# Optimization experiments

Hardware: AMD Instinct MI355X
Metric: run time of the kernel (lower is better)

The kernel has to match this reference:

```python
import jax, jax.numpy as jnp
import numpy as np

NUM_JOINTS = 140
NUM_VERTICES = 13059
NUM_BONES = 28
BATCH = 512


def euler_zyx_to_rot(e):
    """e: [..., 3] Euler angles in (z, y, x) order -> [..., 3, 3] with R = Rz @ Ry @ Rx."""
    z, y, x = e[..., 0], e[..., 1], e[..., 2]
    cx, sx = jnp.cos(x), jnp.sin(x)
    cy, sy = jnp.cos(y), jnp.sin(y)
    cz, sz = jnp.cos(z), jnp.sin(z)
    r00 = cz * cy
    r01 = cz * sy * sx - sz * cx
    r02 = cz * sy * cx + sz * sx
    r10 = sz * cy
    r11 = sz * sy * sx + cz * cx
    r12 = sz * sy * cx - cz * sx
    r20 = -sy
    r21 = cy * sx
    r22 = cy * cx
    R = jnp.stack([r00, r01, r02, r10, r11, r12, r20, r21, r22], axis=-1)
    return R.reshape(e.shape[:-1] + (3, 3))


def _mouse_forward(pose, bone_lengths, center_bone_length, trans, scale,
                   v_template, t_pose_joints, weights, parent, bone_mapper):
    B = pose.shape[0]
    Jn = NUM_JOINTS
    dt = pose.dtype

    bl = jax.nn.sigmoid(bone_lengths / 5.0) * 2.0            # [B, 28]
    R = euler_zyx_to_rot(pose.reshape(B, Jn, 3))             # [B, J, 3, 3]
    Jt = t_pose_joints                                       # [J, 3]

    # bone offsets for joints 1..J-1, scaled per bone_length_mapper
    off = Jt[1:] - Jt[parent[1:]]                            # [J-1, 3]
    blid = bone_mapper[1:]                                   # [J-1]
    bl_g = jnp.where(blid[None, :] >= 0,
                     jnp.take(bl, jnp.maximum(blid, 0), axis=1),
                     jnp.ones((), dt))                       # [B, J-1]
    # joint index 1 (position 0 in the [J-1] arrays) uses center_bone_length
    scale_per = bl_g.at[:, 0].set(center_bone_length[:, 0])
    off_b = off[None] * scale_per[..., None]                 # [B, J-1, 3]

    bottom = jnp.broadcast_to(jnp.array([0., 0., 0., 1.], dt), (B, Jn - 1, 1, 4))
    top = jnp.concatenate([R[:, 1:], off_b[..., None]], axis=-1)   # [B, J-1, 3, 4]
    A = jnp.concatenate([top, bottom], axis=-2)              # [B, J-1, 4, 4] local transforms

    root_t = jnp.broadcast_to(Jt[0], (B, 3))[..., None]      # [B, 3, 1]
    root_top = jnp.concatenate([R[:, 0], root_t], axis=-1)   # [B, 3, 4]
    root_bot = jnp.broadcast_to(jnp.array([0., 0., 0., 1.], dt), (B, 1, 4))
    G0 = jnp.concatenate([root_top, root_bot], axis=-2)      # [B, 4, 4]

    G_init = jnp.zeros((B, Jn, 4, 4), dt).at[:, 0].set(G0)

    def step(G, xs):
        i, p, Ai = xs                                        # Ai: [B, 4, 4]
        Gp = jnp.take(G, p, axis=1)                          # [B, 4, 4]
        Gi = Gp @ Ai
        return G.at[:, i].set(Gi), None

    idx = jnp.arange(1, Jn)
    G, _ = jax.lax.scan(step, G_init, (idx, parent[1:], jnp.swapaxes(A, 0, 1)))

    J_final = G[:, :, :3, 3]                                 # [B, J, 3]

    # subtract rest-pose joint contribution (relative transforms for LBS)
    Jh = jnp.concatenate([jnp.broadcast_to(Jt, (B, Jn, 3)),
                          jnp.zeros((B, Jn, 1), dt)], axis=-1)      # [B, J, 4]
    d = jnp.einsum('bjmn,bjn->bjm', G, Jh)                   # [B, J, 4]
    G_rel = jnp.concatenate([G[..., :3], (G[..., 3] - d)[..., None]], axis=-1)

    # linear blend skinning
    T = jnp.einsum('vj,bjmn->bvmn', weights, G_rel)          # [B, V, 4, 4]
    vh = jnp.concatenate([v_template, jnp.ones((NUM_VERTICES, 1), dt)], axis=-1)
    V = jnp.einsum('bvmn,vn->bvm', T[:, :, :3, :], vh)       # [B, V, 3]

    s = scale[:, 0][:, None, None]
    V = V * s + trans[:, None, :]
    J_out = J_final * s + trans[:, None, :]
    return V, J_out


def setup_inputs() -> dict:
    key = jax.random.key(0)
    ks = jax.random.split(key, 8)
    rng = np.random.default_rng(0)
    parent = np.zeros(NUM_JOINTS, dtype=np.int32)
    for i in range(1, NUM_JOINTS):
        parent[i] = rng.integers(0, i)                       # valid kinematic tree
    bone_mapper = rng.integers(-1, NUM_BONES, size=NUM_JOINTS).astype(np.int32)
    W = jax.random.uniform(ks[6], (NUM_VERTICES, NUM_JOINTS), jnp.float32)
    W = W / jnp.sum(W, axis=1, keepdims=True)                # row-stochastic skinning weights
    return {
        'pose': jax.random.normal(ks[0], (BATCH, NUM_JOINTS * 3), jnp.float32) * 0.2,
        'bone_lengths': jax.random.normal(ks[1], (BATCH, NUM_BONES), jnp.float32),
        'center_bone_length': jax.random.uniform(ks[2], (BATCH, 1), jnp.float32, 0.5, 1.5),
        'trans': jax.random.normal(ks[3], (BATCH, 3), jnp.float32),
        'scale': jax.random.uniform(ks[4], (BATCH, 1), jnp.float32, 0.5, 1.5),
        'v_template': jax.random.normal(ks[5], (NUM_VERTICES, 3), jnp.float32),
        't_pose_joints': jax.random.normal(ks[7], (NUM_JOINTS, 3), jnp.float32),
        'weights': W,
        'parent': jnp.asarray(parent),
        'bone_mapper': jnp.asarray(bone_mapper),
    }


def reference(pose, bone_lengths, center_bone_length, trans, scale,
              v_template, t_pose_joints, weights, parent, bone_mapper):
    return _mouse_forward(pose, bone_lengths, center_bone_length, trans, scale,
                          v_template, t_pose_joints, weights, parent, bone_mapper)
```

## Files before the change

### kernel.cpp

```cpp
#include <hip/hip_runtime.h>
#include <math.h>

#define NJ 140
#define NV 13059
#define NB 512
#define NBONES 28

#define MTILES 103
#define NBLK 12
#define KS 18
#define GRID_GEMM (MTILES*NBLK)

#define APREP_SLOTS (MTILES*KS*512)
#define APREP_PER_XCD 252

typedef _Float16 f16x8 __attribute__((ext_vector_type(8)));
typedef float    f32x4 __attribute__((ext_vector_type(4)));

#define GL16(gp, lp) __builtin_amdgcn_global_load_lds( \
    (const __attribute__((address_space(1))) unsigned int*)(gp), \
    (__attribute__((address_space(3))) unsigned int*)(lp), 16, 0, 0)

__global__ __launch_bounds__(256) void prep_kernel(
    const float* __restrict__ pose,
    const float* __restrict__ bone_lengths,
    const float* __restrict__ cbl,
    const float* __restrict__ trans,
    const float* __restrict__ scale,
    const float* __restrict__ v_template,
    const float* __restrict__ t_pose,
    const int*   __restrict__ parent,
    const int*   __restrict__ bone_mapper,
    const float* __restrict__ weights,
    _Float16* __restrict__ Ap,
    _Float16* __restrict__ Bp,
    float* __restrict__ jout)
{
    const int t = threadIdx.x;

    if (blockIdx.x >= NB) {
        const int r  = blockIdx.x - NB;
        const int x  = r & 7;
        const int l  = r >> 3;
        const int start = x < 4 ? x*155 : 620 + (x-4)*154;
        const int end   = x < 4 ? start + 155 : start + 154;
        const int mlo = (start - 6 + 11) / 12;
        const int mhi = (end   - 6 + 11) / 12;
        const int mt  = mlo + l / KS;
        if (mt >= mhi) return;
        const int ks  = l - (l / KS) * KS;
        const int id  = mt*KS + ks;

        const int row = t >> 1;
        const int q   = t & 1;
        const int v   = mt*128 + row;
        const int j0  = ks*8 + q*4;
        const int s   = (row >> 1) & 3;

        f16x8 oA, oB;
        #pragma unroll
        for (int i = 0; i < 8; ++i) { oA[i] = (_Float16)0.f; oB[i] = (_Float16)0.f; }

        if (v < NV && j0 + 3 < NJ) {
            float xv = v_template[v*3+0];
            float yv = v_template[v*3+1];
            float zv = v_template[v*3+2];
            const float4 w4 = *(const float4*)(weights + (size_t)v*NJ + j0);
            oA[0] = (_Float16)(w4.x*xv); oA[1] = (_Float16)(w4.x*yv);
            oA[2] = (_Float16)(w4.x*zv); oA[3] = (_Float16)w4.x;
            oA[4] = (_Float16)(w4.y*xv); oA[5] = (_Float16)(w4.y*yv);
            oA[6] = (_Float16)(w4.y*zv); oA[7] = (_Float16)w4.y;
            oB[0] = (_Float16)(w4.z*xv); oB[1] = (_Float16)(w4.z*yv);
            oB[2] = (_Float16)(w4.z*zv); oB[3] = (_Float16)w4.z;
            oB[4] = (_Float16)(w4.w*xv); oB[5] = (_Float16)(w4.w*yv);
            oB[6] = (_Float16)(w4.w*zv); oB[7] = (_Float16)w4.w;
        }
        const int base = ((2*q) ^ s) & ~1;
        _Float16* dst = Ap + (((size_t)id)*512 + row*4 + base)*8;
        if (s & 1) {
            *(f16x8*)dst       = oB;
            *(f16x8*)(dst + 8) = oA;
        } else {
            *(f16x8*)dst       = oA;
            *(f16x8*)(dst + 8) = oB;
        }
        return;
    }

    __shared__ float M0[NJ][12];
    __shared__ float M1[NJ][12];
    __shared__ int   a0[NJ];
    __shared__ int   a1[NJ];

    const int b = blockIdx.x;

    if (t < NJ) {
        const int j = t;
        float z = pose[b*(NJ*3) + 3*j + 0];
        float y = pose[b*(NJ*3) + 3*j + 1];
        float x = pose[b*(NJ*3) + 3*j + 2];
        float cx = cosf(x), sx = sinf(x);
        float cy = cosf(y), sy = sinf(y);
        float cz = cosf(z), sz = sinf(z);
        float r00 = cz*cy;
        float r01 = cz*sy*sx - sz*cx;
        float r02 = cz*sy*cx + sz*sx;
        float r10 = sz*cy;
        float r11 = sz*sy*sx + cz*cx;
        float r12 = sz*sy*cx - cz*sx;
        float r20 = -sy;
        float r21 = cy*sx;
        float r22 = cy*cx;
        float t0, t1, t2;
        int p = parent[j];
        if (j == 0) {
            t0 = t_pose[0]; t1 = t_pose[1]; t2 = t_pose[2];
        } else {
            float ox = t_pose[3*j+0] - t_pose[3*p+0];
            float oy = t_pose[3*j+1] - t_pose[3*p+1];
            float oz = t_pose[3*j+2] - t_pose[3*p+2];
            float s;
            if (j == 1) {
                s = cbl[b];
            } else {
                int blid = bone_mapper[j];
                if (blid >= 0) {
                    float bv = bone_lengths[b*NBONES + blid];
                    s = 2.0f / (1.0f + expf(-bv*0.2f));
                } else {
                    s = 1.0f;
                }
            }
            t0 = ox*s; t1 = oy*s; t2 = oz*s;
        }
        M0[j][0]=r00; M0[j][1]=r01; M0[j][2]=r02;  M0[j][3]=t0;
        M0[j][4]=r10; M0[j][5]=r11; M0[j][6]=r12;  M0[j][7]=t1;
        M0[j][8]=r20; M0[j][9]=r21; M0[j][10]=r22; M0[j][11]=t2;
        a0[j] = (j == 0) ? -1 : p;
    }
    __syncthreads();

    float* src = &M0[0][0]; float* dst = &M1[0][0];
    int* as = a0; int* ad = a1;
    for (int r = 0; r < 8; ++r) {
        if (t < NJ) {
            int a = as[t];
            const float* Mi = src + t*12;
            float* Do = dst + t*12;
            if (a >= 0) {
                const float* Mp = src + a*12;
                #pragma unroll
                for (int m = 0; m < 3; ++m) {
                    float p0 = Mp[m*4+0], p1 = Mp[m*4+1], p2 = Mp[m*4+2], p3 = Mp[m*4+3];
                    Do[m*4+0] = p0*Mi[0] + p1*Mi[4] + p2*Mi[8];
                    Do[m*4+1] = p0*Mi[1] + p1*Mi[5] + p2*Mi[9];
                    Do[m*4+2] = p0*Mi[2] + p1*Mi[6] + p2*Mi[10];
                    Do[m*4+3] = p0*Mi[3] + p1*Mi[7] + p2*Mi[11] + p3;
                }
                ad[t] = as[a];
            } else {
                #pragma unroll
                for (int e = 0; e < 12; ++e) Do[e] = Mi[e];
                ad[t] = -1;
            }
        }
        __syncthreads();
        float* tf = src; src = dst; dst = tf;
        int* ti = as; as = ad; ad = ti;
    }

    float* grl = dst;
    if (t < NJ) {
        const int j = t;
        const float* G = src + j*12;
        float sb = scale[b];
        float tr0 = trans[b*3+0], tr1 = trans[b*3+1], tr2 = trans[b*3+2];
        float* jo = jout + ((size_t)b*NJ + j)*3;
        jo[0] = G[3]*sb  + tr0;
        jo[1] = G[7]*sb  + tr1;
        jo[2] = G[11]*sb + tr2;
        float jx = t_pose[3*j+0], jy = t_pose[3*j+1], jz = t_pose[3*j+2];
        #pragma unroll
        for (int c = 0; c < 3; ++c) {
            float g0 = G[c*4+0], g1 = G[c*4+1], g2 = G[c*4+2];
            float g3 = G[c*4+3] - (g0*jx + g1*jy + g2*jz);
            grl[j*12 + c*4 + 0] = g0;
            grl[j*12 + c*4 + 1] = g1;
            grl[j*12 + c*4 + 2] = g2;
            grl[j*12 + c*4 + 3] = g3;
        }
    }
    __syncthreads();

    if (t < 216) {
        int c  = t / 72;
        int rr = t - c*72;
        int ks = rr >> 2;
        int ci = rr & 3;
        int nrow = b*3 + c;
        int nbp = nrow >> 7;
        int rl = nrow & 127;
        int j0 = ks*8 + ci*2;
        f16x8 o;
        #pragma unroll
        for (int i = 0; i < 8; ++i) o[i] = (_Float16)0.f;
        if (j0 < NJ) {
            o[0] = (_Float16)grl[j0*12 + c*4 + 0];
            o[1] = (_Float16)grl[j0*12 + c*4 + 1];
            o[2] = (_Float16)grl[j0*12 + c*4 + 2];
            o[3] = (_Float16)grl[j0*12 + c*4 + 3];
        }
        if (j0 + 1 < NJ) {
            o[4] = (_Float16)grl[(j0+1)*12 + c*4 + 0];
            o[5] = (_Float16)grl[(j0+1)*12 + c*4 + 1];
            o[6] = (_Float16)grl[(j0+1)*12 + c*4 + 2];
            o[7] = (_Float16)grl[(j0+1)*12 + c*4 + 3];
        }
        int cs = ci ^ ((rl >> 1) & 3);
        *(f16x8*)(Bp + ((size_t)(nbp*KS + ks)*512 + rl*4 + cs)*8) = o;
    }
}

__global__ __launch_bounds__(512, 6) void gemm_kernel(
    const _Float16* __restrict__ Ap,
    const _Float16* __restrict__ Bp,
    const float* __restrict__ scale,
    const float* __restrict__ trans,
    float* __restrict__ vout)
{
    __shared__ __align__(16) char smem[40960];
    _Float16 (*sA)[4096] = (_Float16(*)[4096])smem;
    _Float16 (*sB)[4096] = (_Float16(*)[4096])(smem + 24576);

    const int t    = threadIdx.x;
    const int lane = t & 63;
    const int wid  = t >> 6;
    const int ln   = lane & 15;
    const int kq   = lane >> 4;
    const int wm   = wid & 1;
    const int wn   = wid >> 1;

    const int q8 = GRID_GEMM >> 3;
    const int r8 = GRID_GEMM & 7;
    const int xcd = blockIdx.x & 7;
    const int idx = blockIdx.x >> 3;
    const int wgid = (xcd < r8 ? xcd*(q8+1) : r8*(q8+1) + (xcd-r8)*q8) + idx;

    const int mt = wgid / NBLK;
    const int nb = wgid - mt*NBLK;

    const _Float16* Ag = Ap + (size_t)mt*(KS*4096);
    const _Float16* Bg = Bp + (size_t)nb*(KS*4096);

    const int csl = kq ^ ((ln >> 1) & 3);
    const int afo = (wm*64 + ln)*32 + csl*8;
    const int bfo = (wn*32 + ln)*32 + csl*8;

    f32x4 acc[4][2];
    #pragma unroll
    for (int mi = 0; mi < 4; ++mi)
        #pragma unroll
        for (int ni = 0; ni < 2; ++ni)
            acc[mi][ni] = (f32x4){0.f, 0.f, 0.f, 0.f};

    #define STAGE_A(buf, ksv) GL16(Ag + (ksv)*4096 + t*8, &sA[buf][wid*512])
    #define STAGE_B(buf, ksv) GL16(Bg + (ksv)*4096 + t*8, &sB[buf][wid*512])

    auto compute = [&](int ba, int bb) {
        f16x8 af[4], bf[2];
        #pragma unroll
        for (int mi = 0; mi < 4; ++mi)
            af[mi] = *(const f16x8*)&sA[ba][afo + mi*512];
        #pragma unroll
        for (int ni = 0; ni < 2; ++ni)
            bf[ni] = *(const f16x8*)&sB[bb][bfo + ni*512];
        __builtin_amdgcn_s_setprio(1);
        #pragma unroll
        for (int mi = 0; mi < 4; ++mi)
            #pragma unroll
            for (int ni = 0; ni < 2; ++ni)
                acc[mi][ni] = __builtin_amdgcn_mfma_f32_16x16x32_f16(
                    af[mi], bf[ni], acc[mi][ni], 0, 0, 0);
        __builtin_amdgcn_s_setprio(0);
    };

    #define STEP(j, bBn, bAn, bAc, bBc) do { \
        asm volatile("s_waitcnt vmcnt(1)" ::: "memory"); \
        __builtin_amdgcn_s_barrier(); \
        STAGE_B(bBn, (j) + 1); \
        STAGE_A(bAn, (j) + 2); \
        compute(bAc, bBc); } while (0)

    STAGE_B(0, 0);
    STAGE_A(0, 0);
    STAGE_A(1, 1);

    #pragma unroll 1
    for (int i = 0; i < 12; i += 6) {
        STEP(i + 0, 1, 2, 0, 0);
        STEP(i + 1, 0, 0, 1, 1);
        STEP(i + 2, 1, 1, 2, 0);
        STEP(i + 3, 0, 2, 0, 1);
        STEP(i + 4, 1, 0, 1, 0);
        STEP(i + 5, 0, 1, 2, 1);
    }
    STEP(12, 1, 2, 0, 0);
    STEP(13, 0, 0, 1, 1);
    STEP(14, 1, 1, 2, 0);
    STEP(15, 0, 2, 0, 1);
    asm volatile("s_waitcnt vmcnt(1)" ::: "memory");
    __builtin_amdgcn_s_barrier();
    STAGE_B(1, 17);
    compute(1, 0);
    asm volatile("s_waitcnt vmcnt(0)" ::: "memory");
    __builtin_amdgcn_s_barrier();
    compute(2, 1);

    #undef STEP
    #undef STAGE_A
    #undef STAGE_B

    float* Ct    = (float*)smem;
    float* es_l  = (float*)(smem + 33792);
    float* etr_l = (float*)(smem + 34304);

    const int vgA = t/3, crA = t - 3*vgA;

    #pragma unroll 1
    for (int h = 0; h < 2; ++h) {
        __syncthreads();
        if ((wn >> 1) == h) {
            #pragma unroll
            for (int mi = 0; mi < 4; ++mi)
                #pragma unroll
                for (int ni = 0; ni < 2; ++ni)
                    *(f32x4*)&Ct[((wn&1)*32 + ni*16 + ln)*132
                                 + wm*64 + mi*16 + kq*4] = acc[mi][ni];
        }
        if (h == 0 && t < 128) {
            int n = nb*128 + t;
            es_l[t]  = scale[n/3];
            etr_l[t] = trans[n];
        }
        __syncthreads();

        const int n0   = nb*128 + h*64;
        const int bq0  = n0/3;
        const int off0 = 3*bq0 - n0;
        const int bqN  = (n0 + 63)/3 - bq0 + 1;

        #pragma unroll 1
        for (int bqi = 0; bqi < bqN; ++bqi) {
            const long long base = (long long)(bq0 + bqi)*(NV*3)
                                 + (long long)mt*384;
            if (t < 384) {
                int nrel = off0 + 3*bqi + crA;
                if (nrel >= 0 && nrel < 64 && mt*128 + vgA < NV) {
                    int nf = h*64 + nrel;
                    vout[base + t] =
                        Ct[nrel*132 + vgA]*es_l[nf] + etr_l[nf];
                }
            }
        }
    }
}

extern "C" void kernel_launch(void* const* d_in, const int* in_sizes, int n_in,
                              void* d_out, int out_size, void* d_ws, size_t ws_size,
                              hipStream_t stream) {
    const float* pose         = (const float*)d_in[0];
    const float* bone_lengths = (const float*)d_in[1];
    const float* cbl          = (const float*)d_in[2];
    const float* trans        = (const float*)d_in[3];
    const float* scale        = (const float*)d_in[4];
    const float* v_template   = (const float*)d_in[5];
    const float* t_pose       = (const float*)d_in[6];
    const float* weights      = (const float*)d_in[7];
    const int*   parent       = (const int*)d_in[8];
    const int*   bone_mapper  = (const int*)d_in[9];

    float* vout = (float*)d_out;
    float* jout = vout + (size_t)NB*NV*3;

    _Float16* Ap = (_Float16*)d_ws;
    _Float16* Bp = Ap + (size_t)APREP_SLOTS*8;

    prep_kernel<<<NB + 8*APREP_PER_XCD, 256, 0, stream>>>(
        pose, bone_lengths, cbl, trans, scale, v_template, t_pose,
        parent, bone_mapper, weights, Ap, Bp, jout);

    gemm_kernel<<<GRID_GEMM, 512, 0, stream>>>(Ap, Bp, scale, trans, vout);
}
```

Baseline: 145.6 us.

## Double K-step per pipeline stage in GEMM and simplify A-prep block mapping

The GEMM main loop now stages two K-slices per pipeline step (9 steps instead of 18), doubling LDS buffers to 80KB and lowering the launch-bound occupancy hint from 6 to 4. This halves the number of barriers and waitcnt syncs per tile at the cost of fewer resident workgroups. The A-prep blocks drop the XCD-aware tile assignment in favour of a plain linear id mapping, which may lose L2 locality between the prep writes and the GEMM reads.

```diff
diff --git a/kernel.cpp b/kernel.cpp
--- a/kernel.cpp
+++ b/kernel.cpp
@@ -9,10 +9,10 @@
 #define MTILES 103
 #define NBLK 12
 #define KS 18
+#define KS2 9
 #define GRID_GEMM (MTILES*NBLK)
 
 #define APREP_SLOTS (MTILES*KS*512)
-#define APREP_PER_XCD 252
 
 typedef _Float16 f16x8 __attribute__((ext_vector_type(8)));
 typedef float    f32x4 __attribute__((ext_vector_type(4)));
@@ -39,18 +39,9 @@
     const int t = threadIdx.x;
 
     if (blockIdx.x >= NB) {
-        const int r  = blockIdx.x - NB;
-        const int x  = r & 7;
-        const int l  = r >> 3;
-        const int start = x < 4 ? x*155 : 620 + (x-4)*154;
-        const int end   = x < 4 ? start + 155 : start + 154;
-        const int mlo = (start - 6 + 11) / 12;
-        const int mhi = (end   - 6 + 11) / 12;
-        const int mt  = mlo + l / KS;
-        if (mt >= mhi) return;
-        const int ks  = l - (l / KS) * KS;
-        const int id  = mt*KS + ks;
-
+        const int id  = blockIdx.x - NB;
+        const int mt  = id / KS;
+        const int ks  = id - mt*KS;
         const int row = t >> 1;
         const int q   = t & 1;
         const int v   = mt*128 + row;
@@ -221,16 +212,16 @@
     }
 }
 
-__global__ __launch_bounds__(512, 6) void gemm_kernel(
+__global__ __launch_bounds__(512, 4) void gemm_kernel(
     const _Float16* __restrict__ Ap,
     const _Float16* __restrict__ Bp,
     const float* __restrict__ scale,
     const float* __restrict__ trans,
     float* __restrict__ vout)
 {
-    __shared__ __align__(16) char smem[40960];
-    _Float16 (*sA)[4096] = (_Float16(*)[4096])smem;
-    _Float16 (*sB)[4096] = (_Float16(*)[4096])(smem + 24576);
+    __shared__ __align__(16) char smem[81920];
+    #define SA(a) ((_Float16*)(smem + (a)*16384))
+    #define SB(b) ((_Float16*)(smem + 49152 + (b)*16384))
 
     const int t    = threadIdx.x;
     const int lane = t & 63;
@@ -263,29 +254,38 @@
         for (int ni = 0; ni < 2; ++ni)
             acc[mi][ni] = (f32x4){0.f, 0.f, 0.f, 0.f};
 
-    #define STAGE_A(buf, ksv) GL16(Ag + (ksv)*4096 + t*8, &sA[buf][wid*512])
-    #define STAGE_B(buf, ksv) GL16(Bg + (ksv)*4096 + t*8, &sB[buf][wid*512])
+    #define STAGE_A(a, j2) do { \
+        GL16(Ag + (2*(j2)  )*4096 + t*8, SA(a) +        wid*512); \
+        GL16(Ag + (2*(j2)+1)*4096 + t*8, SA(a) + 4096 + wid*512); } while (0)
+    #define STAGE_B(bf_, j2) do { \
+        GL16(Bg + (2*(j2)  )*4096 + t*8, SB(bf_) +        wid*512); \
+        GL16(Bg + (2*(j2)+1)*4096 + t*8, SB(bf_) + 4096 + wid*512); } while (0)
 
     auto compute = [&](int ba, int bb) {
-        f16x8 af[4], bf[2];
-        #pragma unroll
-        for (int mi = 0; mi < 4; ++mi)
-            af[mi] = *(const f16x8*)&sA[ba][afo + mi*512];
-        #pragma unroll
-        for (int ni = 0; ni < 2; ++ni)
-            bf[ni] = *(const f16x8*)&sB[bb][bfo + ni*512];
-        __builtin_amdgcn_s_setprio(1);
-        #pragma unroll
-        for (int mi = 0; mi < 4; ++mi)
+        const _Float16* pa = SA(ba);
+        const _Float16* pb = SB(bb);
+        #pragma unroll
+        for (int half = 0; half < 2; ++half) {
+            f16x8 af[4], bf[2];
+            #pragma unroll
+            for (int mi = 0; mi < 4; ++mi)
+                af[mi] = *(const f16x8*)&pa[half*4096 + afo + mi*512];
             #pragma unroll
             for (int ni = 0; ni < 2; ++ni)
-                acc[mi][ni] = __builtin_amdgcn_mfma_f32_16x16x32_f16(
-                    af[mi], bf[ni], acc[mi][ni], 0, 0, 0);
-        __builtin_amdgcn_s_setprio(0);
+                bf[ni] = *(const f16x8*)&pb[half*4096 + bfo + ni*512];
+            __builtin_amdgcn_s_setprio(1);
+            #pragma unroll
+            for (int mi = 0; mi < 4; ++mi)
+                #pragma unroll
+                for (int ni = 0; ni < 2; ++ni)
+                    acc[mi][ni] = __builtin_amdgcn_mfma_f32_16x16x32_f16(
+                        af[mi], bf[ni], acc[mi][ni], 0, 0, 0);
+            __builtin_amdgcn_s_setprio(0);
+        }
     };
 
     #define STEP(j, bBn, bAn, bAc, bBc) do { \
-        asm volatile("s_waitcnt vmcnt(1)" ::: "memory"); \
+        asm volatile("s_waitcnt vmcnt(2)" ::: "memory"); \
         __builtin_amdgcn_s_barrier(); \
         STAGE_B(bBn, (j) + 1); \
         STAGE_A(bAn, (j) + 2); \
@@ -295,26 +295,20 @@
     STAGE_A(0, 0);
     STAGE_A(1, 1);
 
-    #pragma unroll 1
-    for (int i = 0; i < 12; i += 6) {
-        STEP(i + 0, 1, 2, 0, 0);
-        STEP(i + 1, 0, 0, 1, 1);
-        STEP(i + 2, 1, 1, 2, 0);
-        STEP(i + 3, 0, 2, 0, 1);
-        STEP(i + 4, 1, 0, 1, 0);
-        STEP(i + 5, 0, 1, 2, 1);
-    }
-    STEP(12, 1, 2, 0, 0);
-    STEP(13, 0, 0, 1, 1);
-    STEP(14, 1, 1, 2, 0);
-    STEP(15, 0, 2, 0, 1);
-    asm volatile("s_waitcnt vmcnt(1)" ::: "memory");
+    STEP(0, 1, 2, 0, 0);
+    STEP(1, 0, 0, 1, 1);
+    STEP(2, 1, 1, 2, 0);
+    STEP(3, 0, 2, 0, 1);
+    STEP(4, 1, 0, 1, 0);
+    STEP(5, 0, 1, 2, 1);
+    STEP(6, 1, 2, 0, 0);
+    asm volatile("s_waitcnt vmcnt(2)" ::: "memory");
     __builtin_amdgcn_s_barrier();
-    STAGE_B(1, 17);
-    compute(1, 0);
+    STAGE_B(0, 8);
+    compute(1, 1);
     asm volatile("s_waitcnt vmcnt(0)" ::: "memory");
     __builtin_amdgcn_s_barrier();
-    compute(2, 1);
+    compute(2, 0);
 
     #undef STEP
     #undef STAGE_A
@@ -363,6 +357,8 @@
             }
         }
     }
+    #undef SA
+    #undef SB
 }
 
 extern "C" void kernel_launch(void* const* d_in, const int* in_sizes, int n_in,
@@ -385,7 +381,7 @@
     _Float16* Ap = (_Float16*)d_ws;
     _Float16* Bp = Ap + (size_t)APREP_SLOTS*8;
 
-    prep_kernel<<<NB + 8*APREP_PER_XCD, 256, 0, stream>>>(
+    prep_kernel<<<NB + MTILES*KS, 256, 0, stream>>>(
         pose, bone_lengths, cbl, trans, scale, v_template, t_pose,
         parent, bone_mapper, weights, Ap, Bp, jout);
 
```

New measurement: 147.3 us. Within noise of the previous version (+1.2%).
